# Optimization experiments

Measured on AMD Instinct MI355X. Metric: run time of the kernel, lower is better.

The kernel has to match this reference:

```python
import jax, jax.numpy as jnp
import numpy as np

HIDDEN = 1024
NUM_HEADS = 16
HEAD_DIM = HIDDEN // NUM_HEADS
GRID_SIZE = 5
SPLINE_ORDER = 3
NUM_COEF = GRID_SIZE + SPLINE_ORDER  # 8


def make_grid(in_features):
    # efficient-kan default grid: range [-1, 1], extended by spline_order on each side
    h = 2.0 / GRID_SIZE
    g = jnp.arange(-SPLINE_ORDER, GRID_SIZE + SPLINE_ORDER + 1, dtype=jnp.float32) * h - 1.0
    return jnp.broadcast_to(g, (in_features, g.shape[0]))  # (in, G+2k+1)


def b_splines(x, grid):
    # x: (N, in); grid: (in, G+2k+1) -> bases (N, in, G+k)
    x = x[..., None]
    bases = ((x >= grid[:, :-1]) & (x < grid[:, 1:])).astype(x.dtype)
    for k in range(1, SPLINE_ORDER + 1):
        left = (x - grid[:, : -(k + 1)]) / (grid[:, k:-1] - grid[:, : -(k + 1)])
        right = (grid[:, k + 1 :] - x) / (grid[:, k + 1 :] - grid[:, 1:-k])
        bases = left * bases[..., :-1] + right * bases[..., 1:]
    return bases


def kan_linear(x, base_w, spline_w, spline_scaler):
    # x: (..., in); base_w: (out, in); spline_w: (out, in, C); spline_scaler: (out, in)
    in_f = x.shape[-1]
    x2 = x.reshape(-1, in_f)
    base = jax.nn.silu(x2) @ base_w.T
    bases = b_splines(x2, make_grid(in_f))                      # (N, in, C)
    sw = spline_w * spline_scaler[..., None]                    # (out, in, C)
    spline = bases.reshape(x2.shape[0], -1) @ sw.reshape(sw.shape[0], -1).T
    return (base + spline).reshape(*x.shape[:-1], base_w.shape[0])


def apply_rope(x):
    # x: (B, H, S, D); interleaved rotary (lucidrains convention), theta=10000
    d, s = x.shape[-1], x.shape[-2]
    inv_freq = 1.0 / (10000.0 ** (jnp.arange(0, d, 2, dtype=jnp.float32) / d))
    freqs = jnp.arange(s, dtype=jnp.float32)[:, None] * inv_freq[None, :]  # (S, d/2)
    cos = jnp.repeat(jnp.cos(freqs), 2, axis=-1)
    sin = jnp.repeat(jnp.sin(freqs), 2, axis=-1)
    x1, x2 = x[..., 0::2], x[..., 1::2]
    rot = jnp.stack((-x2, x1), axis=-1).reshape(x.shape)
    return x * cos + rot * sin


def setup_inputs() -> dict:
    key = jax.random.key(0)
    ks = jax.random.split(key, 10)
    B, S, H = 2, 2048, HIDDEN
    H3 = 3 * H
    scale = 0.02
    return {
        "q": jax.random.normal(ks[0], (B, S, H), jnp.float32),
        "k": jax.random.normal(ks[1], (B, S, H), jnp.float32),
        "v": jax.random.normal(ks[2], (B, S, H), jnp.float32),
        "attn_mask": jnp.zeros((S, S), jnp.float32),
        "qkv_base_w": jax.random.normal(ks[3], (H3, H3), jnp.float32) * scale,
        "qkv_spline_w": jax.random.normal(ks[4], (H3, H3, NUM_COEF), jnp.float32) * scale,
        "qkv_scaler": jnp.ones((H3, H3), jnp.float32),
        "out_base_w": jax.random.normal(ks[5], (H, H), jnp.float32) * scale,
        "out_spline_w": jax.random.normal(ks[6], (H, H, NUM_COEF), jnp.float32) * scale,
        "out_scaler": jnp.ones((H, H), jnp.float32),
    }


def reference(q, k, v, attn_mask, qkv_base_w, qkv_spline_w, qkv_scaler,
              out_base_w, out_spline_w, out_scaler):
    B, S, H = q.shape
    x = jnp.concatenate((q, k, v), axis=2)                       # (B, S, 3H)
    qkv = kan_linear(x, qkv_base_w, qkv_spline_w, qkv_scaler)    # (B, S, 3H)
    qkv = qkv.reshape(B, S, NUM_HEADS, 3 * HEAD_DIM).transpose(0, 2, 1, 3)
    queries, keys, values = jnp.split(qkv, 3, axis=-1)           # each (B, nh, S, hd)
    queries = apply_rope(queries)
    keys = apply_rope(keys)
    scores = jnp.einsum("bhqd,bhkd->bhqk", queries, keys) / (HEAD_DIM ** 0.5) + attn_mask
    attention = jax.nn.softmax(scores, axis=-1)
    context = jnp.einsum("bhqk,bhkd->bhqd", attention, values)
    context = context.transpose(0, 2, 1, 3).reshape(B, S, H)
    return kan_linear(context, out_base_w, out_spline_w, out_scaler)
```

## Files before the change

### kernel.cpp

```cpp
#include <hip/hip_runtime.h>
#include <hip/hip_bf16.h>
#include <stdint.h>

typedef __bf16 bf16;
typedef __attribute__((ext_vector_type(8))) __bf16 bf16x8;
typedef __attribute__((ext_vector_type(4))) float f32x4;

#define DEVI __device__ __forceinline__

constexpr int BATCH = 2, SEQ = 2048, HID = 1024, NHEAD = 16, HDIM = 64;
constexpr int H3 = 3072;
constexpr int MROWS = BATCH * SEQ;
constexpr int KEXP = 9;
constexpr int K1DIM = H3 * KEXP;
constexpr int K2DIM = HID * KEXP;

constexpr size_t WQ_OFF  = 0;
constexpr size_t AQ_OFF  = 169869312;
constexpr size_t CQ_OFF  = AQ_OFF + 226492416;
constexpr size_t QR_OFF  = CQ_OFF + 50331648;
constexpr size_t KR_OFF  = QR_OFF + 8388608;
constexpr size_t VB_OFF  = KR_OFF + 8388608;
constexpr size_t CTX_OFF = VB_OFF + 8388608;
constexpr size_t A2_OFF  = 0;
constexpr size_t W2_OFF  = 75497472;

DEVI void gld_lds16(const void* g, void* l) {
  __builtin_amdgcn_global_load_lds((const __attribute__((address_space(1))) void*)g,
                                   (__attribute__((address_space(3))) void*)l, 16, 0, 0);
}

#define WAITVM0() asm volatile("s_waitcnt vmcnt(0)" ::: "memory")
#define MEMFENCE() asm volatile("" ::: "memory")
#define BARRIER() do { __builtin_amdgcn_s_barrier(); asm volatile("" ::: "memory"); } while (0)

DEVI void silu_bases(float x, float* o9) {
  o9[0] = x / (1.0f + __expf(-x));
  float g[12];
#pragma unroll
  for (int j = 0; j < 12; ++j) g[j] = (float)(j - 3) * 0.4f - 1.0f;
  float b[11];
#pragma unroll
  for (int j = 0; j < 11; ++j) b[j] = (x >= g[j] && x < g[j + 1]) ? 1.0f : 0.0f;
#pragma unroll
  for (int k = 1; k <= 3; ++k) {
    const float inv = (k == 1) ? 2.5f : (k == 2) ? 1.25f : (1.0f / 1.2f);
#pragma unroll
    for (int j = 0; j + k < 11; ++j) {
      b[j] = (x - g[j]) * inv * b[j] + (g[j + k + 1] - x) * inv * b[j + 1];
    }
  }
#pragma unroll
  for (int c = 0; c < 8; ++c) o9[1 + c] = b[c];
}

__global__ __launch_bounds__(256)
void wprep_kernel(const float* __restrict__ bw, const float* __restrict__ sw,
                  const float* __restrict__ sc, bf16* __restrict__ W, int KK) {
  __shared__ bf16 buf[256 * KEXP];
  const int tid = threadIdx.x;
  const int n = blockIdx.y;
  const int i0 = blockIdx.x * 256;
  const size_t idx = (size_t)n * KK + i0 + tid;
  float base = bw[idx];
  float scal = sc[idx];
  const float4* sp = (const float4*)(sw + idx * 8);
  float4 s0 = sp[0], s1 = sp[1];
  bf16* o = buf + tid * KEXP;
  o[0] = (bf16)base;
  o[1] = (bf16)(s0.x * scal); o[2] = (bf16)(s0.y * scal);
  o[3] = (bf16)(s0.z * scal); o[4] = (bf16)(s0.w * scal);
  o[5] = (bf16)(s1.x * scal); o[6] = (bf16)(s1.y * scal);
  o[7] = (bf16)(s1.z * scal); o[8] = (bf16)(s1.w * scal);
  __syncthreads();
  bf16* dst = W + (size_t)n * KK * KEXP + (size_t)i0 * KEXP;
#pragma unroll
  for (int j = tid; j < 256 * KEXP / 8; j += 256)
    *(bf16x8*)(dst + j * 8) = *(const bf16x8*)(buf + j * 8);
}

__global__ __launch_bounds__(256)
void act_qkv_kernel(const float* __restrict__ qin, const float* __restrict__ kin,
                    const float* __restrict__ vin, bf16* __restrict__ A) {
  __shared__ bf16 buf[256 * KEXP];
  const int tid = threadIdx.x;
  const int m = blockIdx.y;
  const int i0 = blockIdx.x * 256;
  const int i = i0 + tid;
  const int which = i >> 10, off = i & 1023;
  const float* src = (which == 0) ? qin : (which == 1) ? kin : vin;
  float x = src[(size_t)m * HID + off];
  float o9[9];
  silu_bases(x, o9);
  bf16* o = buf + tid * KEXP;
#pragma unroll
  for (int c = 0; c < 9; ++c) o[c] = (bf16)o9[c];
  __syncthreads();
  bf16* dst = A + (size_t)m * K1DIM + (size_t)i0 * KEXP;
#pragma unroll
  for (int j = tid; j < 256 * KEXP / 8; j += 256)
    *(bf16x8*)(dst + j * 8) = *(const bf16x8*)(buf + j * 8);
}

__global__ __launch_bounds__(256)
void act_out_kernel(const float* __restrict__ ctx, bf16* __restrict__ A) {
  __shared__ bf16 buf[256 * KEXP];
  const int tid = threadIdx.x;
  const int m = blockIdx.y;
  const int i0 = blockIdx.x * 256;
  float x = ctx[(size_t)m * HID + i0 + tid];
  float o9[9];
  silu_bases(x, o9);
  bf16* o = buf + tid * KEXP;
#pragma unroll
  for (int c = 0; c < 9; ++c) o[c] = (bf16)o9[c];
  __syncthreads();
  bf16* dst = A + (size_t)m * K2DIM + (size_t)i0 * KEXP;
#pragma unroll
  for (int j = tid; j < 256 * KEXP / 8; j += 256)
    *(bf16x8*)(dst + j * 8) = *(const bf16x8*)(buf + j * 8);
}

__global__ __launch_bounds__(256, 2)
void gemm_kernel(const bf16* __restrict__ A, const bf16* __restrict__ Bw,
                 float* __restrict__ C, int N, int K) {
  __shared__ bf16 As[128 * 64];
  __shared__ bf16 Bs[128 * 64];
  const int tid = threadIdx.x;
  const int lane = tid & 63;
  const int l15 = lane & 15, lq = lane >> 4;
  const int wid = tid >> 6;
  const int wm = (wid >> 1) * 64, wn = (wid & 1) * 64;
  const int bm = blockIdx.y, bn = blockIdx.x;
  f32x4 acc[4][4] = {};
  const int srow = tid >> 3;
  const int schk = (tid & 7) ^ (srow & 7);
  const bf16* aB = A + (size_t)(bm * 128 + srow) * K + schk * 8;
  const bf16* bB = Bw + (size_t)(bn * 128 + srow) * K + schk * 8;

  int aoff[2][4], boff[2][4];
#pragma unroll
  for (int ks = 0; ks < 2; ++ks) {
#pragma unroll
    for (int f = 0; f < 4; ++f) {
      int arow = wm + f * 16 + l15;
      int brow = wn + f * 16 + l15;
      aoff[ks][f] = arow * 64 + (((ks * 4 + lq) ^ (arow & 7)) * 8);
      boff[ks][f] = brow * 64 + (((ks * 4 + lq) ^ (brow & 7)) * 8);
    }
  }

  for (int kt = 0; kt < K; kt += 64) {
#pragma unroll
    for (int r = 0; r < 4; ++r) {
      gld_lds16(aB + (size_t)(r * 32) * K + kt, As + r * 2048 + tid * 8);
      gld_lds16(bB + (size_t)(r * 32) * K + kt, Bs + r * 2048 + tid * 8);
    }
    __syncthreads();
#pragma unroll
    for (int ks = 0; ks < 2; ++ks) {
      bf16x8 af[4], bfr[4];
#pragma unroll
      for (int mf = 0; mf < 4; ++mf)
        af[mf] = *(const bf16x8*)&As[aoff[ks][mf]];
#pragma unroll
      for (int nf = 0; nf < 4; ++nf)
        bfr[nf] = *(const bf16x8*)&Bs[boff[ks][nf]];
#pragma unroll
      for (int mf = 0; mf < 4; ++mf)
#pragma unroll
        for (int nf = 0; nf < 4; ++nf)
          acc[mf][nf] = __builtin_amdgcn_mfma_f32_16x16x32_bf16(af[mf], bfr[nf], acc[mf][nf], 0, 0, 0);
    }
    __syncthreads();
  }
#pragma unroll
  for (int mf = 0; mf < 4; ++mf)
#pragma unroll
    for (int nf = 0; nf < 4; ++nf)
#pragma unroll
      for (int r = 0; r < 4; ++r) {
        int row = bm * 128 + wm + mf * 16 + lq * 4 + r;
        int col = bn * 128 + wn + nf * 16 + l15;
        C[(size_t)row * N + col] = acc[mf][nf][r];
      }
}

__global__ void rope_kernel(const float* __restrict__ Cq, bf16* __restrict__ qr,
                            bf16* __restrict__ kr, bf16* __restrict__ vt) {
  int idx = blockIdx.x * blockDim.x + threadIdx.x;
  int p = idx & 31;
  int h = (idx >> 5) & 15;
  int m = idx >> 9;
  int s = m & (SEQ - 1);
  int b = m >> 11;
  const float* row = Cq + (size_t)m * H3 + h * 192;
  float q0 = row[2 * p], q1 = row[2 * p + 1];
  float k0 = row[64 + 2 * p], k1 = row[64 + 2 * p + 1];
  float v0 = row[128 + 2 * p], v1 = row[128 + 2 * p + 1];
  float invf = expf(-(float)p * (9.210340371976184f / 32.0f));
  float fr = (float)s * invf;
  float sn, cs;
  sincosf(fr, &sn, &cs);
  const int bh = b * NHEAD + h;
  size_t o = ((size_t)bh * SEQ + s) * 64 + 2 * p;
  qr[o] = (bf16)((q0 * cs - q1 * sn) * 0.125f);
  qr[o + 1] = (bf16)((q1 * cs + q0 * sn) * 0.125f);
  kr[o] = (bf16)(k0 * cs - k1 * sn); kr[o + 1] = (bf16)(k1 * cs + k0 * sn);
  vt[((size_t)bh * 64 + 2 * p) * SEQ + s] = (bf16)v0;
  vt[((size_t)bh * 64 + 2 * p + 1) * SEQ + s] = (bf16)v1;
}

__global__ __launch_bounds__(256, 2)
void attn_kernel(const bf16* __restrict__ qr, const bf16* __restrict__ kr,
                 const bf16* __restrict__ vt, const float* __restrict__ mask,
                 float* __restrict__ ctx) {
  __shared__ bf16 Kt[2][64 * 64];
  __shared__ bf16 Vt[2][64 * 64];
  __shared__ bf16 Pl[4][16 * 64];
  const int tid = threadIdx.x, lane = tid & 63, wid = tid >> 6;
  const int l15 = lane & 15, lq = lane >> 4;
  const int qt = blockIdx.x, bh = blockIdx.y;
  const int b = bh >> 4, hh = bh & 15;
  const size_t baseQ = ((size_t)bh * SEQ + qt * 64 + wid * 16) * 64;
  bf16x8 aq[2];
  aq[0] = *(const bf16x8*)&qr[baseQ + (size_t)l15 * 64 + 0 + lq * 8];
  aq[1] = *(const bf16x8*)&qr[baseQ + (size_t)l15 * 64 + 32 + lq * 8];
  float mrow[4], lrow[4];
  f32x4 oacc[4] = {};
#pragma unroll
  for (int r = 0; r < 4; ++r) { mrow[r] = -1e30f; lrow[r] = 0.0f; }
  const int srow = tid >> 3;
  const int schk = (tid & 7) ^ (srow & 7);
  const bf16* kBase = kr + ((size_t)bh * SEQ + srow) * 64 + schk * 8;
  const bf16* vBase = vt + ((size_t)bh * 64 + srow) * SEQ + schk * 8;

#define ASTAGE(bi_, kv_)                                                        \
  do {                                                                          \
    gld_lds16(kBase + (size_t)(kv_) * 64, &Kt[bi_][0] + tid * 8);               \
    gld_lds16(kBase + (size_t)((kv_) + 32) * 64, &Kt[bi_][0] + 2048 + tid * 8); \
    gld_lds16(vBase + (kv_), &Vt[bi_][0] + tid * 8);                            \
    gld_lds16(vBase + (size_t)32 * SEQ + (kv_), &Vt[bi_][0] + 2048 + tid * 8);  \
  } while (0)

  ASTAGE(0, 0);
  WAITVM0();
  BARRIER();
  for (int kv0 = 0; kv0 < SEQ; kv0 += 64) {
    const int cur = (kv0 >> 6) & 1;
    if (kv0 + 64 < SEQ) { ASTAGE(cur ^ 1, kv0 + 64); MEMFENCE(); }
    const bf16* kt = &Kt[cur][0];
    const bf16* vtl = &Vt[cur][0];
    f32x4 sacc[4] = {};
#pragma unroll
    for (int k0 = 0; k0 < 2; ++k0) {
#pragma unroll
      for (int nf = 0; nf < 4; ++nf) {
        bf16x8 bk = *(const bf16x8*)&kt[(nf * 16 + l15) * 64 + (((k0 * 4 + lq) ^ (l15 & 7)) << 3)];
        sacc[nf] = __builtin_amdgcn_mfma_f32_16x16x32_bf16(aq[k0], bk, sacc[nf], 0, 0, 0);
      }
    }
    const int qg0 = qt * 64 + wid * 16 + lq * 4;
#pragma unroll
    for (int nf = 0; nf < 4; ++nf) {
      int kvg = kv0 + nf * 16 + l15;
#pragma unroll
      for (int r = 0; r < 4; ++r)
        sacc[nf][r] += mask[(size_t)(qg0 + r) * SEQ + kvg];
    }
    float fac[4];
#pragma unroll
    for (int r = 0; r < 4; ++r) {
      float v = fmaxf(fmaxf(sacc[0][r], sacc[1][r]), fmaxf(sacc[2][r], sacc[3][r]));
      v = fmaxf(v, __shfl_xor(v, 1));
      v = fmaxf(v, __shfl_xor(v, 2));
      v = fmaxf(v, __shfl_xor(v, 4));
      v = fmaxf(v, __shfl_xor(v, 8));
      float mnew = fmaxf(mrow[r], v);
      fac[r] = __expf(mrow[r] - mnew);
      mrow[r] = mnew;
    }
    float rs[4] = {0, 0, 0, 0};
#pragma unroll
    for (int nf = 0; nf < 4; ++nf)
#pragma unroll
      for (int r = 0; r < 4; ++r) {
        float pv = __expf(sacc[nf][r] - mrow[r]);
        sacc[nf][r] = pv;
        rs[r] += pv;
      }
#pragma unroll
    for (int r = 0; r < 4; ++r) {
      float v = rs[r];
      v += __shfl_xor(v, 1); v += __shfl_xor(v, 2);
      v += __shfl_xor(v, 4); v += __shfl_xor(v, 8);
      lrow[r] = lrow[r] * fac[r] + v;
    }
#pragma unroll
    for (int nf = 0; nf < 4; ++nf)
#pragma unroll
      for (int r = 0; r < 4; ++r) {
        int qrow = lq * 4 + r;
        int col = nf * 16 + l15;
        Pl[wid][qrow * 64 + ((((col >> 3) ^ (qrow & 7))) << 3) + (col & 7)] = (bf16)sacc[nf][r];
      }
#pragma unroll
    for (int nf = 0; nf < 4; ++nf)
#pragma unroll
      for (int r = 0; r < 4; ++r)
        oacc[nf][r] *= fac[r];
#pragma unroll
    for (int k0 = 0; k0 < 2; ++k0) {
      bf16x8 ap = *(const bf16x8*)&Pl[wid][l15 * 64 + (((k0 * 4 + lq) ^ (l15 & 7)) << 3)];
#pragma unroll
      for (int nf = 0; nf < 4; ++nf) {
        bf16x8 bv = *(const bf16x8*)&vtl[(nf * 16 + l15) * 64 + (((k0 * 4 + lq) ^ (l15 & 7)) << 3)];
        oacc[nf] = __builtin_amdgcn_mfma_f32_16x16x32_bf16(ap, bv, oacc[nf], 0, 0, 0);
      }
    }
    WAITVM0();
    BARRIER();
  }
#undef ASTAGE
#pragma unroll
  for (int nf = 0; nf < 4; ++nf)
#pragma unroll
    for (int r = 0; r < 4; ++r) {
      int row = qt * 64 + wid * 16 + lq * 4 + r;
      int col = hh * 64 + nf * 16 + l15;
      ctx[((size_t)b * SEQ + row) * HID + col] = oacc[nf][r] / lrow[r];
    }
}

extern "C" void kernel_launch(void* const* d_in, const int* in_sizes, int n_in,
                              void* d_out, int out_size, void* d_ws, size_t ws_size,
                              hipStream_t stream) {
  const float* qin    = (const float*)d_in[0];
  const float* kin    = (const float*)d_in[1];
  const float* vin    = (const float*)d_in[2];
  const float* mask   = (const float*)d_in[3];
  const float* qkv_bw = (const float*)d_in[4];
  const float* qkv_sw = (const float*)d_in[5];
  const float* qkv_sc = (const float*)d_in[6];
  const float* out_bw = (const float*)d_in[7];
  const float* out_sw = (const float*)d_in[8];
  const float* out_sc = (const float*)d_in[9];
  char* ws = (char*)d_ws;
  bf16* Wq  = (bf16*)(ws + WQ_OFF);
  bf16* Aq  = (bf16*)(ws + AQ_OFF);
  float* Cq = (float*)(ws + CQ_OFF);
  bf16* qr  = (bf16*)(ws + QR_OFF);
  bf16* kr  = (bf16*)(ws + KR_OFF);
  bf16* vt  = (bf16*)(ws + VB_OFF);
  float* ctx = (float*)(ws + CTX_OFF);
  bf16* A2  = (bf16*)(ws + A2_OFF);
  bf16* W2  = (bf16*)(ws + W2_OFF);

  wprep_kernel<<<dim3(H3 / 256, H3), 256, 0, stream>>>(qkv_bw, qkv_sw, qkv_sc, Wq, H3);
  act_qkv_kernel<<<dim3(H3 / 256, MROWS), 256, 0, stream>>>(qin, kin, vin, Aq);
  gemm_kernel<<<dim3(H3 / 128, MROWS / 128), 256, 0, stream>>>(Aq, Wq, Cq, H3, K1DIM);
  rope_kernel<<<(MROWS * NHEAD * 32) / 256, 256, 0, stream>>>(Cq, qr, kr, vt);
  attn_kernel<<<dim3(SEQ / 64, BATCH * NHEAD), 256, 0, stream>>>(qr, kr, vt, mask, ctx);
  act_out_kernel<<<dim3(HID / 256, MROWS), 256, 0, stream>>>(ctx, A2);
  wprep_kernel<<<dim3(HID / 256, HID), 256, 0, stream>>>(out_bw, out_sw, out_sc, W2, HID);
  gemm_kernel<<<dim3(HID / 128, MROWS / 128), 256, 0, stream>>>(A2, W2, (float*)d_out, HID, K2DIM);
}
```

Before: 1.151 ms.

## Convert mask to bf16, add 64-row tile GEMM for output, set MFMA priority

Adds a prep kernel that converts the fp32 attention mask to bf16, so the attention kernel reads half the mask bytes on every KV tile. It also adds a 64x128-tile GEMM for the output projection, doubling the block count for the smaller N=1024 GEMM to fill more CUs. s_setprio is raised around the MFMA sections of the attention loop. The bf16 mask loses precision for arbitrary mask values and adds an extra pass over the mask.

```diff
diff --git a/kernel.cpp b/kernel.cpp
--- a/kernel.cpp
+++ b/kernel.cpp
@@ -3,6 +3,7 @@
 #include <stdint.h>
 
 typedef __bf16 bf16;
+typedef __attribute__((ext_vector_type(4))) __bf16 bf16x4;
 typedef __attribute__((ext_vector_type(8))) __bf16 bf16x8;
 typedef __attribute__((ext_vector_type(4))) float f32x4;
 
@@ -24,6 +25,7 @@
 constexpr size_t CTX_OFF = VB_OFF + 8388608;
 constexpr size_t A2_OFF  = 0;
 constexpr size_t W2_OFF  = 75497472;
+constexpr size_t MB_OFF  = W2_OFF + 18874368;
 
 DEVI void gld_lds16(const void* g, void* l) {
   __builtin_amdgcn_global_load_lds((const __attribute__((address_space(1))) void*)g,
@@ -121,6 +123,14 @@
     *(bf16x8*)(dst + j * 8) = *(const bf16x8*)(buf + j * 8);
 }
 
+__global__ __launch_bounds__(256)
+void maskprep_kernel(const float* __restrict__ m, bf16* __restrict__ mb) {
+  int i = (blockIdx.x * 256 + threadIdx.x) * 4;
+  float4 v = *(const float4*)(m + i);
+  bf16x4 o = { (bf16)v.x, (bf16)v.y, (bf16)v.z, (bf16)v.w };
+  *(bf16x4*)(mb + i) = o;
+}
+
 __global__ __launch_bounds__(256, 2)
 void gemm_kernel(const bf16* __restrict__ A, const bf16* __restrict__ Bw,
                  float* __restrict__ C, int N, int K) {
@@ -182,6 +192,75 @@
       for (int r = 0; r < 4; ++r) {
         int row = bm * 128 + wm + mf * 16 + lq * 4 + r;
         int col = bn * 128 + wn + nf * 16 + l15;
+        C[(size_t)row * N + col] = acc[mf][nf][r];
+      }
+}
+
+__global__ __launch_bounds__(256, 2)
+void gemm2_kernel(const bf16* __restrict__ A, const bf16* __restrict__ Bw,
+                  float* __restrict__ C, int N, int K) {
+  __shared__ bf16 As[64 * 64];
+  __shared__ bf16 Bs[128 * 64];
+  const int tid = threadIdx.x;
+  const int lane = tid & 63;
+  const int l15 = lane & 15, lq = lane >> 4;
+  const int wid = tid >> 6;
+  const int wr = wid >> 1, wc = wid & 1;
+  const int bm = blockIdx.y, bn = blockIdx.x;
+  f32x4 acc[2][4] = {};
+  const int srow = tid >> 3;
+  const int schk = (tid & 7) ^ (srow & 7);
+  const bf16* aB = A + (size_t)(bm * 64 + srow) * K + schk * 8;
+  const bf16* bB = Bw + (size_t)(bn * 128 + srow) * K + schk * 8;
+
+  int aoff[2][2], boff[2][4];
+#pragma unroll
+  for (int ks = 0; ks < 2; ++ks) {
+#pragma unroll
+    for (int f = 0; f < 2; ++f) {
+      int arow = wr * 32 + f * 16 + l15;
+      aoff[ks][f] = arow * 64 + (((ks * 4 + lq) ^ (arow & 7)) * 8);
+    }
+#pragma unroll
+    for (int f = 0; f < 4; ++f) {
+      int brow = wc * 64 + f * 16 + l15;
+      boff[ks][f] = brow * 64 + (((ks * 4 + lq) ^ (brow & 7)) * 8);
+    }
+  }
+
+  for (int kt = 0; kt < K; kt += 64) {
+#pragma unroll
+    for (int r = 0; r < 2; ++r)
+      gld_lds16(aB + (size_t)(r * 32) * K + kt, As + r * 2048 + tid * 8);
+#pragma unroll
+    for (int r = 0; r < 4; ++r)
+      gld_lds16(bB + (size_t)(r * 32) * K + kt, Bs + r * 2048 + tid * 8);
+    __syncthreads();
+#pragma unroll
+    for (int ks = 0; ks < 2; ++ks) {
+      bf16x8 af[2], bfr[4];
+#pragma unroll
+      for (int mf = 0; mf < 2; ++mf)
+        af[mf] = *(const bf16x8*)&As[aoff[ks][mf]];
+#pragma unroll
+      for (int nf = 0; nf < 4; ++nf)
+        bfr[nf] = *(const bf16x8*)&Bs[boff[ks][nf]];
+#pragma unroll
+      for (int mf = 0; mf < 2; ++mf)
+#pragma unroll
+        for (int nf = 0; nf < 4; ++nf)
+          acc[mf][nf] = __builtin_amdgcn_mfma_f32_16x16x32_bf16(af[mf], bfr[nf], acc[mf][nf], 0, 0, 0);
+    }
+    __syncthreads();
+  }
+#pragma unroll
+  for (int mf = 0; mf < 2; ++mf)
+#pragma unroll
+    for (int nf = 0; nf < 4; ++nf)
+#pragma unroll
+      for (int r = 0; r < 4; ++r) {
+        int row = bm * 64 + wr * 32 + mf * 16 + lq * 4 + r;
+        int col = bn * 128 + wc * 64 + nf * 16 + l15;
         C[(size_t)row * N + col] = acc[mf][nf][r];
       }
 }
@@ -213,7 +292,7 @@
 
 __global__ __launch_bounds__(256, 2)
 void attn_kernel(const bf16* __restrict__ qr, const bf16* __restrict__ kr,
-                 const bf16* __restrict__ vt, const float* __restrict__ mask,
+                 const bf16* __restrict__ vt, const bf16* __restrict__ maskb,
                  float* __restrict__ ctx) {
   __shared__ bf16 Kt[2][64 * 64];
   __shared__ bf16 Vt[2][64 * 64];
@@ -252,6 +331,7 @@
     const bf16* kt = &Kt[cur][0];
     const bf16* vtl = &Vt[cur][0];
     f32x4 sacc[4] = {};
+    __builtin_amdgcn_s_setprio(1);
 #pragma unroll
     for (int k0 = 0; k0 < 2; ++k0) {
 #pragma unroll
@@ -260,13 +340,14 @@
         sacc[nf] = __builtin_amdgcn_mfma_f32_16x16x32_bf16(aq[k0], bk, sacc[nf], 0, 0, 0);
       }
     }
+    __builtin_amdgcn_s_setprio(0);
     const int qg0 = qt * 64 + wid * 16 + lq * 4;
 #pragma unroll
     for (int nf = 0; nf < 4; ++nf) {
       int kvg = kv0 + nf * 16 + l15;
 #pragma unroll
       for (int r = 0; r < 4; ++r)
-        sacc[nf][r] += mask[(size_t)(qg0 + r) * SEQ + kvg];
+        sacc[nf][r] += (float)maskb[(size_t)(qg0 + r) * SEQ + kvg];
     }
     float fac[4];
 #pragma unroll
@@ -309,6 +390,7 @@
 #pragma unroll
       for (int r = 0; r < 4; ++r)
         oacc[nf][r] *= fac[r];
+    __builtin_amdgcn_s_setprio(1);
 #pragma unroll
     for (int k0 = 0; k0 < 2; ++k0) {
       bf16x8 ap = *(const bf16x8*)&Pl[wid][l15 * 64 + (((k0 * 4 + lq) ^ (l15 & 7)) << 3)];
@@ -318,6 +400,7 @@
         oacc[nf] = __builtin_amdgcn_mfma_f32_16x16x32_bf16(ap, bv, oacc[nf], 0, 0, 0);
       }
     }
+    __builtin_amdgcn_s_setprio(0);
     WAITVM0();
     BARRIER();
   }
@@ -355,13 +438,15 @@
   float* ctx = (float*)(ws + CTX_OFF);
   bf16* A2  = (bf16*)(ws + A2_OFF);
   bf16* W2  = (bf16*)(ws + W2_OFF);
+  bf16* mb  = (bf16*)(ws + MB_OFF);
 
   wprep_kernel<<<dim3(H3 / 256, H3), 256, 0, stream>>>(qkv_bw, qkv_sw, qkv_sc, Wq, H3);
   act_qkv_kernel<<<dim3(H3 / 256, MROWS), 256, 0, stream>>>(qin, kin, vin, Aq);
   gemm_kernel<<<dim3(H3 / 128, MROWS / 128), 256, 0, stream>>>(Aq, Wq, Cq, H3, K1DIM);
+  maskprep_kernel<<<(SEQ * SEQ) / 1024, 256, 0, stream>>>(mask, mb);
   rope_kernel<<<(MROWS * NHEAD * 32) / 256, 256, 0, stream>>>(Cq, qr, kr, vt);
-  attn_kernel<<<dim3(SEQ / 64, BATCH * NHEAD), 256, 0, stream>>>(qr, kr, vt, mask, ctx);
+  attn_kernel<<<dim3(SEQ / 64, BATCH * NHEAD), 256, 0, stream>>>(qr, kr, vt, mb, ctx);
   act_out_kernel<<<dim3(HID / 256, MROWS), 256, 0, stream>>>(ctx, A2);
   wprep_kernel<<<dim3(HID / 256, HID), 256, 0, stream>>>(out_bw, out_sw, out_sc, W2, HID);
-  gemm_kernel<<<dim3(HID / 128, MROWS / 128), 256, 0, stream>>>(A2, W2, (float*)d_out, HID, K2DIM);
-}
+  gemm2_kernel<<<dim3(HID / 128, MROWS / 64), 256, 0, stream>>>(A2, W2, (float*)d_out, HID, K2DIM);
+}
```

After: 1.119 ms. 1.03x faster.
